# Kernel optimization log

Hardware: AMD Instinct MI355X
Metric: run time of the kernel (lower is better)

## Reference

```python
import jax, jax.numpy as jnp
import numpy as np

B, T, I, D, O = 256, 512, 64, 512, 128
LN_EPS = 1e-5


def setup_inputs() -> dict:
    key = jax.random.key(0)
    ks = jax.random.split(key, 4)
    x = jax.random.normal(ks[0], (B, T, I), dtype=jnp.float32)
    W_in = jax.random.normal(ks[1], (D, I), dtype=jnp.float32) * (1.0 / np.sqrt(I))
    b_in = jnp.zeros((D,), dtype=jnp.float32)
    gamma = jnp.ones((D,), dtype=jnp.float32)
    beta = jnp.zeros((D,), dtype=jnp.float32)
    W_out = jax.random.normal(ks[2], (O, D), dtype=jnp.float32) * (1.0 / np.sqrt(D))
    b_out = jnp.zeros((O,), dtype=jnp.float32)
    context_strength = jnp.float32(0.2)
    return {"x": x, "W_in": W_in, "b_in": b_in, "gamma": gamma, "beta": beta,
            "W_out": W_out, "b_out": b_out, "context_strength": context_strength}


def reference(x, W_in, b_in, gamma, beta, W_out, b_out, context_strength):
    # memory_ring slot 0 is the only one ever read/written, so context_read at
    # step t is simply state_update from step t-1 (zeros at t=0).
    b, t, _ = x.shape
    d = W_in.shape[0]
    # Precompute all input embeddings in one GEMM: [B,T,D]
    e = jnp.tanh(jnp.einsum('bti,di->btd', x, W_in) + b_in)
    scale = jax.nn.sigmoid(context_strength)

    def layer_norm(s):
        mu = jnp.mean(s, axis=-1, keepdims=True)
        var = jnp.mean((s - mu) ** 2, axis=-1, keepdims=True)
        return (s - mu) * jax.lax.rsqrt(var + LN_EPS) * gamma + beta

    def step(carry, e_t):
        s_prev, h_prev = carry  # state_update_{t-1}, hidden_{t-1}
        s = jnp.tanh(e_t + scale * s_prev + h_prev)
        h = layer_norm(s)
        return (s, h), None

    init = (jnp.zeros((b, d), dtype=x.dtype), jnp.zeros((b, d), dtype=x.dtype))
    (_, h_final), _ = jax.lax.scan(step, init, jnp.swapaxes(e, 0, 1))  # scan over T
    logits = h_final @ W_out.T + b_out  # [B,O]
    return logits
```

## Files before the change

### kernel.cpp

```cpp
#include <hip/hip_runtime.h>

#define BB 256
#define TT 512
#define II 64
#define DD 512
#define OO 128
#define LN_EPS 1e-5f
#define XS_STRIDE 68

__device__ __forceinline__ float fast_tanh(float x) {
    float e = __expf(2.0f * x);
    return 1.0f - 2.0f / (e + 1.0f);
}

__global__ __launch_bounds__(256, 4)
void embed_kernel(const float* __restrict__ x,
                  const float* __restrict__ W_in,
                  const float* __restrict__ b_in,
                  float* __restrict__ E,
                  int t0, int CT)
{
    __shared__ float xs[II][XS_STRIDE];
    __shared__ float ws[II][XS_STRIDE];

    const int tiles_per_b = CT >> 6;
    const int bx   = blockIdx.x;
    const int b    = bx / tiles_per_b;
    const int tau0 = (bx - b * tiles_per_b) << 6;
    const int d0   = blockIdx.y << 6;
    const int tid  = threadIdx.x;

    {
        const int r0 = tid >> 4;
        const int c4 = tid & 15;
        #pragma unroll
        for (int rr = 0; rr < 4; ++rr) {
            const int row = r0 + (rr << 4);
            const float4 xv = *(const float4*)(x + ((size_t)(b * TT + t0 + tau0 + row)) * II + c4 * 4);
            const float4 wv = *(const float4*)(W_in + ((size_t)(d0 + row)) * II + c4 * 4);
            xs[c4 * 4 + 0][row] = xv.x; xs[c4 * 4 + 1][row] = xv.y;
            xs[c4 * 4 + 2][row] = xv.z; xs[c4 * 4 + 3][row] = xv.w;
            ws[c4 * 4 + 0][row] = wv.x; ws[c4 * 4 + 1][row] = wv.y;
            ws[c4 * 4 + 2][row] = wv.z; ws[c4 * 4 + 3][row] = wv.w;
        }
    }
    __syncthreads();

    const int tn = tid & 15;
    const int td = tid >> 4;

    float acc[4][4];
    #pragma unroll
    for (int j = 0; j < 4; ++j)
        #pragma unroll
        for (int k = 0; k < 4; ++k) acc[j][k] = 0.0f;

    #pragma unroll 8
    for (int i = 0; i < II; ++i) {
        const float4 xv = *(const float4*)&xs[i][tn * 4];
        const float4 wv = *(const float4*)&ws[i][td * 4];
        acc[0][0] = fmaf(xv.x, wv.x, acc[0][0]);
        acc[0][1] = fmaf(xv.x, wv.y, acc[0][1]);
        acc[0][2] = fmaf(xv.x, wv.z, acc[0][2]);
        acc[0][3] = fmaf(xv.x, wv.w, acc[0][3]);
        acc[1][0] = fmaf(xv.y, wv.x, acc[1][0]);
        acc[1][1] = fmaf(xv.y, wv.y, acc[1][1]);
        acc[1][2] = fmaf(xv.y, wv.z, acc[1][2]);
        acc[1][3] = fmaf(xv.y, wv.w, acc[1][3]);
        acc[2][0] = fmaf(xv.z, wv.x, acc[2][0]);
        acc[2][1] = fmaf(xv.z, wv.y, acc[2][1]);
        acc[2][2] = fmaf(xv.z, wv.z, acc[2][2]);
        acc[2][3] = fmaf(xv.z, wv.w, acc[2][3]);
        acc[3][0] = fmaf(xv.w, wv.x, acc[3][0]);
        acc[3][1] = fmaf(xv.w, wv.y, acc[3][1]);
        acc[3][2] = fmaf(xv.w, wv.z, acc[3][2]);
        acc[3][3] = fmaf(xv.w, wv.w, acc[3][3]);
    }

    const int dg = d0 + td * 4;
    const float4 bv = *(const float4*)(b_in + dg);
    #pragma unroll
    for (int j = 0; j < 4; ++j) {
        const int n = tau0 + tn * 4 + j;
        float4 ev;
        ev.x = fast_tanh(acc[j][0] + bv.x);
        ev.y = fast_tanh(acc[j][1] + bv.y);
        ev.z = fast_tanh(acc[j][2] + bv.z);
        ev.w = fast_tanh(acc[j][3] + bv.w);
        *(float4*)(E + ((size_t)(b * CT + n)) * DD + dg) = ev;
    }
}

__global__ __launch_bounds__(512, 2)
void recur_kernel(const float* __restrict__ E,
                  const float* __restrict__ gamma,
                  const float* __restrict__ beta,
                  const float* __restrict__ W_out,
                  const float* __restrict__ b_out,
                  const float* __restrict__ cs,
                  float* __restrict__ s_state,
                  float* __restrict__ h_state,
                  float* __restrict__ out,
                  int CT, int is_first, int is_last)
{
    const int b    = blockIdx.x;
    const int tid  = threadIdx.x;
    const int wave = tid >> 6;
    const int lane = tid & 63;

    __shared__ float red[2][8][2];
    __shared__ float h_lds[DD];

    const float g  = gamma[tid];
    const float bt = beta[tid];
    const float scale = 1.0f / (1.0f + __expf(-cs[0]));

    float s_prev, h_prev;
    if (is_first) { s_prev = 0.0f; h_prev = 0.0f; }
    else {
        s_prev = s_state[(size_t)b * DD + tid];
        h_prev = h_state[(size_t)b * DD + tid];
    }

    const float* Eb = E + (size_t)b * CT * DD;
    float e0 = Eb[tid];
    float e1 = Eb[(size_t)DD + tid];

    #pragma unroll 1
    for (int tau = 0; tau < CT; ++tau) {
        const int tpre = (tau + 2 < CT) ? tau + 2 : CT - 1;
        const float e2 = Eb[(size_t)tpre * DD + tid];

        const float s = fast_tanh(e0 + scale * s_prev + h_prev);

        float r0 = s, r1 = s * s;
        #pragma unroll
        for (int m = 32; m >= 1; m >>= 1) {
            r0 += __shfl_xor(r0, m, 64);
            r1 += __shfl_xor(r1, m, 64);
        }
        const int p = tau & 1;
        if (lane == 0) { red[p][wave][0] = r0; red[p][wave][1] = r1; }
        __syncthreads();

        float sum = 0.f, sumsq = 0.f;
        #pragma unroll
        for (int wv = 0; wv < 8; ++wv) {
            sum   += red[p][wv][0];
            sumsq += red[p][wv][1];
        }

        const float mu   = sum * (1.0f / DD);
        const float var  = sumsq * (1.0f / DD) - mu * mu;
        const float rstd = rsqrtf(var + LN_EPS);
        const float h    = (s - mu) * rstd * g + bt;

        s_prev = s;
        h_prev = h;
        e0 = e1;
        e1 = e2;
    }

    if (!is_last) {
        s_state[(size_t)b * DD + tid] = s_prev;
        h_state[(size_t)b * DD + tid] = h_prev;
    } else {
        h_lds[tid] = h_prev;
        __syncthreads();

        const int dbase = lane * 8;
        float hreg[8];
        #pragma unroll
        for (int k = 0; k < 8; ++k) hreg[k] = h_lds[dbase + k];

        for (int oo = 0; oo < 16; ++oo) {
            const int o = wave * 16 + oo;
            const float* wo = W_out + (size_t)o * DD + dbase;
            float pacc = 0.f;
            #pragma unroll
            for (int k = 0; k < 8; ++k) pacc = fmaf(wo[k], hreg[k], pacc);
            #pragma unroll
            for (int m = 32; m >= 1; m >>= 1) pacc += __shfl_xor(pacc, m, 64);
            if (lane == 0) out[(size_t)b * OO + o] = pacc + b_out[o];
        }
    }
}

extern "C" void kernel_launch(void* const* d_in, const int* in_sizes, int n_in,
                              void* d_out, int out_size, void* d_ws, size_t ws_size,
                              hipStream_t stream) {
    const float* x      = (const float*)d_in[0];
    const float* W_in   = (const float*)d_in[1];
    const float* b_in   = (const float*)d_in[2];
    const float* gamma  = (const float*)d_in[3];
    const float* beta   = (const float*)d_in[4];
    const float* W_out  = (const float*)d_in[5];
    const float* b_out  = (const float*)d_in[6];
    const float* cs     = (const float*)d_in[7];
    float* out = (float*)d_out;

    const size_t state_bytes = (size_t)BB * DD * sizeof(float);
    int CT = TT;
    while (CT > 64 &&
           (size_t)BB * CT * DD * sizeof(float) + 2 * state_bytes > ws_size) {
        CT >>= 1;
    }
    float* E       = (float*)d_ws;
    float* s_state = (float*)((char*)d_ws + (size_t)BB * CT * DD * sizeof(float));
    float* h_state = s_state + (size_t)BB * DD;

    const int nchunks = TT / CT;
    for (int c = 0; c < nchunks; ++c) {
        dim3 g1(BB * (CT >> 6), DD >> 6);
        embed_kernel<<<g1, 256, 0, stream>>>(x, W_in, b_in, E, c * CT, CT);
        recur_kernel<<<BB, 512, 0, stream>>>(E, gamma, beta, W_out, b_out, cs,
                                             s_state, h_state, out, CT,
                                             (c == 0) ? 1 : 0,
                                             (c == nchunks - 1) ? 1 : 0);
    }
}
```

Baseline: 502.4 us.

## Run recurrence with one wavefront per batch row to drop block barriers

The recurrence kernel now uses a single 64-lane wavefront per batch element, with each lane owning 8 contiguous features loaded as float4 pairs. Layer-norm statistics come from wave shuffles alone, so the per-timestep LDS write and __syncthreads are gone. The cost is 8x fewer threads in flight: 256 waves on the whole GPU, so the many transcendental ops and loads per lane per step run serially with less latency hiding. The output projection is also done by that single wave.

```diff
diff --git a/kernel.cpp b/kernel.cpp
--- a/kernel.cpp
+++ b/kernel.cpp
@@ -91,7 +91,7 @@
     }
 }
 
-__global__ __launch_bounds__(512, 2)
+__global__ __launch_bounds__(64, 1)
 void recur_kernel(const float* __restrict__ E,
                   const float* __restrict__ gamma,
                   const float* __restrict__ beta,
@@ -103,85 +103,93 @@
                   float* __restrict__ out,
                   int CT, int is_first, int is_last)
 {
-    const int b    = blockIdx.x;
-    const int tid  = threadIdx.x;
-    const int wave = tid >> 6;
-    const int lane = tid & 63;
-
-    __shared__ float red[2][8][2];
-    __shared__ float h_lds[DD];
-
-    const float g  = gamma[tid];
-    const float bt = beta[tid];
+    const int b     = blockIdx.x;
+    const int lane  = threadIdx.x;
+    const int dbase = lane << 3;
+
+    const float4 ga = *(const float4*)(gamma + dbase);
+    const float4 gb = *(const float4*)(gamma + dbase + 4);
+    const float4 za = *(const float4*)(beta  + dbase);
+    const float4 zb = *(const float4*)(beta  + dbase + 4);
+
     const float scale = 1.0f / (1.0f + __expf(-cs[0]));
 
-    float s_prev, h_prev;
-    if (is_first) { s_prev = 0.0f; h_prev = 0.0f; }
-    else {
-        s_prev = s_state[(size_t)b * DD + tid];
-        h_prev = h_state[(size_t)b * DD + tid];
-    }
-
-    const float* Eb = E + (size_t)b * CT * DD;
-    float e0 = Eb[tid];
-    float e1 = Eb[(size_t)DD + tid];
+    float4 spa, spb, hpa, hpb;
+    if (is_first) {
+        spa.x = spa.y = spa.z = spa.w = 0.0f;
+        spb = spa; hpa = spa; hpb = spa;
+    } else {
+        spa = *(const float4*)(s_state + (size_t)b * DD + dbase);
+        spb = *(const float4*)(s_state + (size_t)b * DD + dbase + 4);
+        hpa = *(const float4*)(h_state + (size_t)b * DD + dbase);
+        hpb = *(const float4*)(h_state + (size_t)b * DD + dbase + 4);
+    }
+
+    const float* Eb = E + (size_t)b * CT * DD + dbase;
+
+    float4 e0a = *(const float4*)(Eb);
+    float4 e0b = *(const float4*)(Eb + 4);
+    float4 e1a = *(const float4*)(Eb + DD);
+    float4 e1b = *(const float4*)(Eb + DD + 4);
 
     #pragma unroll 1
     for (int tau = 0; tau < CT; ++tau) {
         const int tpre = (tau + 2 < CT) ? tau + 2 : CT - 1;
-        const float e2 = Eb[(size_t)tpre * DD + tid];
-
-        const float s = fast_tanh(e0 + scale * s_prev + h_prev);
-
-        float r0 = s, r1 = s * s;
+        const float4 e2a = *(const float4*)(Eb + (size_t)tpre * DD);
+        const float4 e2b = *(const float4*)(Eb + (size_t)tpre * DD + 4);
+
+        float4 sa, sb;
+        sa.x = fast_tanh(e0a.x + scale * spa.x + hpa.x);
+        sa.y = fast_tanh(e0a.y + scale * spa.y + hpa.y);
+        sa.z = fast_tanh(e0a.z + scale * spa.z + hpa.z);
+        sa.w = fast_tanh(e0a.w + scale * spa.w + hpa.w);
+        sb.x = fast_tanh(e0b.x + scale * spb.x + hpb.x);
+        sb.y = fast_tanh(e0b.y + scale * spb.y + hpb.y);
+        sb.z = fast_tanh(e0b.z + scale * spb.z + hpb.z);
+        sb.w = fast_tanh(e0b.w + scale * spb.w + hpb.w);
+
+        float r0 = ((sa.x + sa.y) + (sa.z + sa.w)) + ((sb.x + sb.y) + (sb.z + sb.w));
+        float r1 = ((sa.x * sa.x + sa.y * sa.y) + (sa.z * sa.z + sa.w * sa.w))
+                 + ((sb.x * sb.x + sb.y * sb.y) + (sb.z * sb.z + sb.w * sb.w));
         #pragma unroll
         for (int m = 32; m >= 1; m >>= 1) {
             r0 += __shfl_xor(r0, m, 64);
             r1 += __shfl_xor(r1, m, 64);
         }
-        const int p = tau & 1;
-        if (lane == 0) { red[p][wave][0] = r0; red[p][wave][1] = r1; }
-        __syncthreads();
-
-        float sum = 0.f, sumsq = 0.f;
-        #pragma unroll
-        for (int wv = 0; wv < 8; ++wv) {
-            sum   += red[p][wv][0];
-            sumsq += red[p][wv][1];
-        }
-
-        const float mu   = sum * (1.0f / DD);
-        const float var  = sumsq * (1.0f / DD) - mu * mu;
+
+        const float mu   = r0 * (1.0f / DD);
+        const float var  = r1 * (1.0f / DD) - mu * mu;
         const float rstd = rsqrtf(var + LN_EPS);
-        const float h    = (s - mu) * rstd * g + bt;
-
-        s_prev = s;
-        h_prev = h;
-        e0 = e1;
-        e1 = e2;
+
+        hpa.x = (sa.x - mu) * rstd * ga.x + za.x;
+        hpa.y = (sa.y - mu) * rstd * ga.y + za.y;
+        hpa.z = (sa.z - mu) * rstd * ga.z + za.z;
+        hpa.w = (sa.w - mu) * rstd * ga.w + za.w;
+        hpb.x = (sb.x - mu) * rstd * gb.x + zb.x;
+        hpb.y = (sb.y - mu) * rstd * gb.y + zb.y;
+        hpb.z = (sb.z - mu) * rstd * gb.z + zb.z;
+        hpb.w = (sb.w - mu) * rstd * gb.w + zb.w;
+
+        spa = sa; spb = sb;
+        e0a = e1a; e0b = e1b;
+        e1a = e2a; e1b = e2b;
     }
 
     if (!is_last) {
-        s_state[(size_t)b * DD + tid] = s_prev;
-        h_state[(size_t)b * DD + tid] = h_prev;
+        *(float4*)(s_state + (size_t)b * DD + dbase)     = spa;
+        *(float4*)(s_state + (size_t)b * DD + dbase + 4) = spb;
+        *(float4*)(h_state + (size_t)b * DD + dbase)     = hpa;
+        *(float4*)(h_state + (size_t)b * DD + dbase + 4) = hpb;
     } else {
-        h_lds[tid] = h_prev;
-        __syncthreads();
-
-        const int dbase = lane * 8;
-        float hreg[8];
-        #pragma unroll
-        for (int k = 0; k < 8; ++k) hreg[k] = h_lds[dbase + k];
-
-        for (int oo = 0; oo < 16; ++oo) {
-            const int o = wave * 16 + oo;
+        for (int o = 0; o < OO; ++o) {
             const float* wo = W_out + (size_t)o * DD + dbase;
-            float pacc = 0.f;
+            const float4 wa = *(const float4*)(wo);
+            const float4 wb = *(const float4*)(wo + 4);
+            float p = wa.x * hpa.x + wa.y * hpa.y + wa.z * hpa.z + wa.w * hpa.w
+                    + wb.x * hpb.x + wb.y * hpb.y + wb.z * hpb.z + wb.w * hpb.w;
             #pragma unroll
-            for (int k = 0; k < 8; ++k) pacc = fmaf(wo[k], hreg[k], pacc);
-            #pragma unroll
-            for (int m = 32; m >= 1; m >>= 1) pacc += __shfl_xor(pacc, m, 64);
-            if (lane == 0) out[(size_t)b * OO + o] = pacc + b_out[o];
+            for (int m = 32; m >= 1; m >>= 1) p += __shfl_xor(p, m, 64);
+            if (lane == 0) out[(size_t)b * OO + o] = p + b_out[o];
         }
     }
 }
@@ -213,9 +221,9 @@
     for (int c = 0; c < nchunks; ++c) {
         dim3 g1(BB * (CT >> 6), DD >> 6);
         embed_kernel<<<g1, 256, 0, stream>>>(x, W_in, b_in, E, c * CT, CT);
-        recur_kernel<<<BB, 512, 0, stream>>>(E, gamma, beta, W_out, b_out, cs,
-                                             s_state, h_state, out, CT,
-                                             (c == 0) ? 1 : 0,
-                                             (c == nchunks - 1) ? 1 : 0);
-    }
-}
+        recur_kernel<<<BB, 64, 0, stream>>>(E, gamma, beta, W_out, b_out, cs,
+                                            s_state, h_state, out, CT,
+                                            (c == 0) ? 1 : 0,
+                                            (c == nchunks - 1) ? 1 : 0);
+    }
+}
```

New measurement: 725.6 us. 1.44x slower.

## Widen embed GEMM tile to 128 columns and halve recurrence block to 256 threads

Applied to the files above, without the earlier changes.

The embedding GEMM tile grows from 64 to 128 output features per block, with each thread computing a 4x8 register tile. This cuts how often x is reloaded and halves the grid's y dimension. The recurrence kernel now uses 256 threads, each owning two features through float2 loads. That halves the per-step cross-wave reduction to 4 waves and makes the barrier cheaper, but each thread does more serial work per step and the embed kernel may run at lower occupancy.

```diff
diff --git a/kernel.cpp b/kernel.cpp
--- a/kernel.cpp
+++ b/kernel.cpp
@@ -7,13 +7,14 @@
 #define OO 128
 #define LN_EPS 1e-5f
 #define XS_STRIDE 68
+#define WS_STRIDE 132
 
 __device__ __forceinline__ float fast_tanh(float x) {
     float e = __expf(2.0f * x);
     return 1.0f - 2.0f / (e + 1.0f);
 }
 
-__global__ __launch_bounds__(256, 4)
+__global__ __launch_bounds__(256, 2)
 void embed_kernel(const float* __restrict__ x,
                   const float* __restrict__ W_in,
                   const float* __restrict__ b_in,
@@ -21,27 +22,29 @@
                   int t0, int CT)
 {
     __shared__ float xs[II][XS_STRIDE];
-    __shared__ float ws[II][XS_STRIDE];
+    __shared__ float ws[II][WS_STRIDE];
 
     const int tiles_per_b = CT >> 6;
     const int bx   = blockIdx.x;
     const int b    = bx / tiles_per_b;
     const int tau0 = (bx - b * tiles_per_b) << 6;
-    const int d0   = blockIdx.y << 6;
+    const int d0   = blockIdx.y << 7;
     const int tid  = threadIdx.x;
 
     {
         const int r0 = tid >> 4;
         const int c4 = tid & 15;
         #pragma unroll
-        for (int rr = 0; rr < 4; ++rr) {
+        for (int rr = 0; rr < 8; ++rr) {
             const int row = r0 + (rr << 4);
-            const float4 xv = *(const float4*)(x + ((size_t)(b * TT + t0 + tau0 + row)) * II + c4 * 4);
             const float4 wv = *(const float4*)(W_in + ((size_t)(d0 + row)) * II + c4 * 4);
-            xs[c4 * 4 + 0][row] = xv.x; xs[c4 * 4 + 1][row] = xv.y;
-            xs[c4 * 4 + 2][row] = xv.z; xs[c4 * 4 + 3][row] = xv.w;
             ws[c4 * 4 + 0][row] = wv.x; ws[c4 * 4 + 1][row] = wv.y;
             ws[c4 * 4 + 2][row] = wv.z; ws[c4 * 4 + 3][row] = wv.w;
+            if (rr < 4) {
+                const float4 xv = *(const float4*)(x + ((size_t)(b * TT + t0 + tau0 + row)) * II + c4 * 4);
+                xs[c4 * 4 + 0][row] = xv.x; xs[c4 * 4 + 1][row] = xv.y;
+                xs[c4 * 4 + 2][row] = xv.z; xs[c4 * 4 + 3][row] = xv.w;
+            }
         }
     }
     __syncthreads();
@@ -49,49 +52,53 @@
     const int tn = tid & 15;
     const int td = tid >> 4;
 
-    float acc[4][4];
+    float acc[4][8];
     #pragma unroll
     for (int j = 0; j < 4; ++j)
         #pragma unroll
-        for (int k = 0; k < 4; ++k) acc[j][k] = 0.0f;
-
-    #pragma unroll 8
+        for (int k = 0; k < 8; ++k) acc[j][k] = 0.0f;
+
+    #pragma unroll 4
     for (int i = 0; i < II; ++i) {
         const float4 xv = *(const float4*)&xs[i][tn * 4];
-        const float4 wv = *(const float4*)&ws[i][td * 4];
-        acc[0][0] = fmaf(xv.x, wv.x, acc[0][0]);
-        acc[0][1] = fmaf(xv.x, wv.y, acc[0][1]);
-        acc[0][2] = fmaf(xv.x, wv.z, acc[0][2]);
-        acc[0][3] = fmaf(xv.x, wv.w, acc[0][3]);
-        acc[1][0] = fmaf(xv.y, wv.x, acc[1][0]);
-        acc[1][1] = fmaf(xv.y, wv.y, acc[1][1]);
-        acc[1][2] = fmaf(xv.y, wv.z, acc[1][2]);
-        acc[1][3] = fmaf(xv.y, wv.w, acc[1][3]);
-        acc[2][0] = fmaf(xv.z, wv.x, acc[2][0]);
-        acc[2][1] = fmaf(xv.z, wv.y, acc[2][1]);
-        acc[2][2] = fmaf(xv.z, wv.z, acc[2][2]);
-        acc[2][3] = fmaf(xv.z, wv.w, acc[2][3]);
-        acc[3][0] = fmaf(xv.w, wv.x, acc[3][0]);
-        acc[3][1] = fmaf(xv.w, wv.y, acc[3][1]);
-        acc[3][2] = fmaf(xv.w, wv.z, acc[3][2]);
-        acc[3][3] = fmaf(xv.w, wv.w, acc[3][3]);
-    }
-
-    const int dg = d0 + td * 4;
-    const float4 bv = *(const float4*)(b_in + dg);
+        const float4 wa = *(const float4*)&ws[i][td * 8];
+        const float4 wb = *(const float4*)&ws[i][td * 8 + 4];
+        #pragma unroll
+        for (int j = 0; j < 4; ++j) {
+            const float xj = (j == 0) ? xv.x : (j == 1) ? xv.y : (j == 2) ? xv.z : xv.w;
+            acc[j][0] = fmaf(xj, wa.x, acc[j][0]);
+            acc[j][1] = fmaf(xj, wa.y, acc[j][1]);
+            acc[j][2] = fmaf(xj, wa.z, acc[j][2]);
+            acc[j][3] = fmaf(xj, wa.w, acc[j][3]);
+            acc[j][4] = fmaf(xj, wb.x, acc[j][4]);
+            acc[j][5] = fmaf(xj, wb.y, acc[j][5]);
+            acc[j][6] = fmaf(xj, wb.z, acc[j][6]);
+            acc[j][7] = fmaf(xj, wb.w, acc[j][7]);
+        }
+    }
+
+    const int dg = d0 + td * 8;
+    const float4 bv0 = *(const float4*)(b_in + dg);
+    const float4 bv1 = *(const float4*)(b_in + dg + 4);
     #pragma unroll
     for (int j = 0; j < 4; ++j) {
         const int n = tau0 + tn * 4 + j;
-        float4 ev;
-        ev.x = fast_tanh(acc[j][0] + bv.x);
-        ev.y = fast_tanh(acc[j][1] + bv.y);
-        ev.z = fast_tanh(acc[j][2] + bv.z);
-        ev.w = fast_tanh(acc[j][3] + bv.w);
-        *(float4*)(E + ((size_t)(b * CT + n)) * DD + dg) = ev;
-    }
-}
-
-__global__ __launch_bounds__(512, 2)
+        float4 e0, e1;
+        e0.x = fast_tanh(acc[j][0] + bv0.x);
+        e0.y = fast_tanh(acc[j][1] + bv0.y);
+        e0.z = fast_tanh(acc[j][2] + bv0.z);
+        e0.w = fast_tanh(acc[j][3] + bv0.w);
+        e1.x = fast_tanh(acc[j][4] + bv1.x);
+        e1.y = fast_tanh(acc[j][5] + bv1.y);
+        e1.z = fast_tanh(acc[j][6] + bv1.z);
+        e1.w = fast_tanh(acc[j][7] + bv1.w);
+        float* dst = E + ((size_t)(b * CT + n)) * DD + dg;
+        *(float4*)(dst)     = e0;
+        *(float4*)(dst + 4) = e1;
+    }
+}
+
+__global__ __launch_bounds__(256)
 void recur_kernel(const float* __restrict__ E,
                   const float* __restrict__ gamma,
                   const float* __restrict__ beta,
@@ -107,65 +114,69 @@
     const int tid  = threadIdx.x;
     const int wave = tid >> 6;
     const int lane = tid & 63;
-
-    __shared__ float red[2][8][2];
+    const int d2   = tid << 1;
+
+    __shared__ __align__(16) float red[2][4][2];
     __shared__ float h_lds[DD];
 
-    const float g  = gamma[tid];
-    const float bt = beta[tid];
+    const float2 g  = *(const float2*)(gamma + d2);
+    const float2 bt = *(const float2*)(beta  + d2);
     const float scale = 1.0f / (1.0f + __expf(-cs[0]));
 
-    float s_prev, h_prev;
-    if (is_first) { s_prev = 0.0f; h_prev = 0.0f; }
+    float2 sp, hp;
+    if (is_first) { sp.x = sp.y = 0.0f; hp = sp; }
     else {
-        s_prev = s_state[(size_t)b * DD + tid];
-        h_prev = h_state[(size_t)b * DD + tid];
+        sp = *(const float2*)(s_state + (size_t)b * DD + d2);
+        hp = *(const float2*)(h_state + (size_t)b * DD + d2);
     }
 
     const float* Eb = E + (size_t)b * CT * DD;
-    float e0 = Eb[tid];
-    float e1 = Eb[(size_t)DD + tid];
+    float2 e0 = *(const float2*)(Eb + d2);
+    float2 e1 = *(const float2*)(Eb + DD + d2);
 
     #pragma unroll 1
     for (int tau = 0; tau < CT; ++tau) {
         const int tpre = (tau + 2 < CT) ? tau + 2 : CT - 1;
-        const float e2 = Eb[(size_t)tpre * DD + tid];
-
-        const float s = fast_tanh(e0 + scale * s_prev + h_prev);
-
-        float r0 = s, r1 = s * s;
+        const float2 e2 = *(const float2*)(Eb + (size_t)tpre * DD + d2);
+
+        float2 s;
+        s.x = fast_tanh(e0.x + scale * sp.x + hp.x);
+        s.y = fast_tanh(e0.y + scale * sp.y + hp.y);
+
+        float r0 = s.x + s.y;
+        float r1 = s.x * s.x + s.y * s.y;
         #pragma unroll
         for (int m = 32; m >= 1; m >>= 1) {
             r0 += __shfl_xor(r0, m, 64);
             r1 += __shfl_xor(r1, m, 64);
         }
+
         const int p = tau & 1;
         if (lane == 0) { red[p][wave][0] = r0; red[p][wave][1] = r1; }
         __syncthreads();
 
-        float sum = 0.f, sumsq = 0.f;
-        #pragma unroll
-        for (int wv = 0; wv < 8; ++wv) {
-            sum   += red[p][wv][0];
-            sumsq += red[p][wv][1];
-        }
+        const float4 ra = *(const float4*)&red[p][0][0];
+        const float4 rb = *(const float4*)&red[p][2][0];
+        const float sum   = (ra.x + ra.z) + (rb.x + rb.z);
+        const float sumsq = (ra.y + ra.w) + (rb.y + rb.w);
 
         const float mu   = sum * (1.0f / DD);
         const float var  = sumsq * (1.0f / DD) - mu * mu;
         const float rstd = rsqrtf(var + LN_EPS);
-        const float h    = (s - mu) * rstd * g + bt;
-
-        s_prev = s;
-        h_prev = h;
+
+        hp.x = (s.x - mu) * rstd * g.x + bt.x;
+        hp.y = (s.y - mu) * rstd * g.y + bt.y;
+        sp = s;
         e0 = e1;
         e1 = e2;
     }
 
     if (!is_last) {
-        s_state[(size_t)b * DD + tid] = s_prev;
-        h_state[(size_t)b * DD + tid] = h_prev;
+        *(float2*)(s_state + (size_t)b * DD + d2) = sp;
+        *(float2*)(h_state + (size_t)b * DD + d2) = hp;
     } else {
-        h_lds[tid] = h_prev;
+        h_lds[d2]     = hp.x;
+        h_lds[d2 + 1] = hp.y;
         __syncthreads();
 
         const int dbase = lane * 8;
@@ -173,8 +184,8 @@
         #pragma unroll
         for (int k = 0; k < 8; ++k) hreg[k] = h_lds[dbase + k];
 
-        for (int oo = 0; oo < 16; ++oo) {
-            const int o = wave * 16 + oo;
+        for (int oo = 0; oo < 32; ++oo) {
+            const int o = wave * 32 + oo;
             const float* wo = W_out + (size_t)o * DD + dbase;
             float pacc = 0.f;
             #pragma unroll
@@ -211,9 +222,9 @@
 
     const int nchunks = TT / CT;
     for (int c = 0; c < nchunks; ++c) {
-        dim3 g1(BB * (CT >> 6), DD >> 6);
+        dim3 g1(BB * (CT >> 6), DD >> 7);
         embed_kernel<<<g1, 256, 0, stream>>>(x, W_in, b_in, E, c * CT, CT);
-        recur_kernel<<<BB, 512, 0, stream>>>(E, gamma, beta, W_out, b_out, cs,
+        recur_kernel<<<BB, 256, 0, stream>>>(E, gamma, beta, W_out, b_out, cs,
                                              s_state, h_state, out, CT,
                                              (c == 0) ? 1 : 0,
                                              (c == nchunks - 1) ? 1 : 0);
```

New measurement: 472.9 us. 5.9% less time.
